# Kernel optimization log

Hardware: AMD Instinct MI355X
Metric: run time of the kernel (lower is better)

Reference implementation:

```python
import jax, jax.numpy as jnp
import numpy as np
from functools import partial

D_MODEL = 1024
D_HIDDEN = 4096
N_BLOCKS = 4
D_VOCAB = 32000
BATCH = 2
SEQ = 2048
LN_EPS = 1e-5
LRELU_SLOPE = 0.01  # torch nn.LeakyReLU default


def setup_inputs() -> dict:
    key = jax.random.key(0)
    ks = jax.random.split(key, 16)
    d, h, L, v = D_MODEL, D_HIDDEN, N_BLOCKS, D_VOCAB
    scale = d ** 0.5
    inp = {
        "tokens": jax.random.randint(ks[0], (BATCH, SEQ), 0, v, dtype=jnp.int64)
                  if jax.config.jax_enable_x64 else
                  jax.random.randint(ks[0], (BATCH, SEQ), 0, v, dtype=jnp.int32),
        "emb": jax.random.normal(ks[1], (v, d), jnp.float32) * 0.02,
        # per-block stacked params (leading axis = layer) for lax.scan
        "qk": jax.random.normal(ks[2], (L, d, d), jnp.float32) / scale,
        "ov": jax.random.normal(ks[3], (L, d, d), jnp.float32) / scale,
        "w_up": jax.random.normal(ks[4], (L, d, h), jnp.float32) / scale,
        "b_up": jnp.zeros((L, h), jnp.float32),
        "w_hid": jax.random.normal(ks[5], (L, h, h), jnp.float32) / (h ** 0.5),
        "b_hid": jnp.zeros((L, h), jnp.float32),
        "w_down": jax.random.normal(ks[6], (L, h, d), jnp.float32) / (h ** 0.5),
        "b_down": jnp.zeros((L, d), jnp.float32),
        "ln1_g": jnp.ones((L, d), jnp.float32),
        "ln1_b": jnp.zeros((L, d), jnp.float32),
        "ln2_g": jnp.ones((L, d), jnp.float32),
        "ln2_b": jnp.zeros((L, d), jnp.float32),
    }
    return inp


def _layer_norm(x, g, b):
    mu = jnp.mean(x, axis=-1, keepdims=True)
    var = jnp.mean(jnp.square(x - mu), axis=-1, keepdims=True)
    return (x - mu) * jax.lax.rsqrt(var + LN_EPS) * g + b


def _forward(tokens, emb, qk, ov, w_up, b_up, w_hid, b_hid, w_down, b_down,
             ln1_g, ln1_b, ln2_g, ln2_b):
    x = emb[tokens]                                   # [B, S, D]
    seq = tokens.shape[1]
    scale = jnp.asarray(D_MODEL ** 0.5, x.dtype)
    causal = jnp.tril(jnp.ones((seq, seq), bool))     # True = keep

    def block(x, p):
        (qk, ov, w_up, b_up, w_hid, b_hid, w_down, b_down,
         g1, b1, g2, b2) = p
        h = _layer_norm(x, g1, b1)
        # attention: (h @ qk @ h^T) / sqrt(d), causal mask, softmax, @ h @ ov
        scores = jnp.einsum('bsd,de,bte->bst', h, qk, h) / scale
        scores = jnp.where(causal, scores, -jnp.inf)
        attn = jax.nn.softmax(scores, axis=-1)
        x = x + jnp.einsum('bst,btd,de->bse', attn, h, ov)
        # MLP with LeakyReLU after every layer (incl. output)
        m = _layer_norm(x, g2, b2)
        m = jax.nn.leaky_relu(m @ w_up + b_up, LRELU_SLOPE)
        m = jax.nn.leaky_relu(m @ w_hid + b_hid, LRELU_SLOPE)
        m = jax.nn.leaky_relu(m @ w_down + b_down, LRELU_SLOPE)
        return x + m, None

    params = (qk, ov, w_up, b_up, w_hid, b_hid, w_down, b_down,
              ln1_g, ln1_b, ln2_g, ln2_b)
    x, _ = jax.lax.scan(block, x, params)
    return x @ emb.T                                  # [B, S, V] logits


@jax.jit
def reference(tokens, emb, qk, ov, w_up, b_up, w_hid, b_hid, w_down, b_down,
              ln1_g, ln1_b, ln2_g, ln2_b):
    return _forward(tokens, emb, qk, ov, w_up, b_up, w_hid, b_hid,
                    w_down, b_down, ln1_g, ln1_b, ln2_g, ln2_b)
```

## Files before the change

### kernel.cpp

```cpp
#include <hip/hip_runtime.h>

#define BS   4096
#define SEQL 2048
#define DM   1024
#define DH   4096
#define NV   32000

using u16 = unsigned short;

typedef __attribute__((ext_vector_type(8))) short bf16x8;
typedef __attribute__((ext_vector_type(4))) float f32x4;

__device__ __forceinline__ u16 f2b(float f) {
  union { float f; unsigned u; } c; c.f = f;
  unsigned u = c.u;
  u = (u + 0x7FFFu + ((u >> 16) & 1u)) >> 16;
  return (u16)u;
}

__device__ __forceinline__ void gld16(const u16* g, u16* l) {
  __builtin_amdgcn_global_load_lds(
      (__attribute__((address_space(1))) void*)(void*)const_cast<u16*>(g),
      (__attribute__((address_space(3))) void*)l, 16, 0, 0);
}

__global__ __launch_bounds__(256) void k_embed(const int* __restrict__ tok,
                                               const float* __restrict__ emb,
                                               float* __restrict__ x) {
  const long row = blockIdx.x;
  const long e = tok[row];
  ((float4*)(x + row * DM))[threadIdx.x] = ((const float4*)(emb + e * DM))[threadIdx.x];
}

__global__ __launch_bounds__(256) void k_cvt(const float* __restrict__ in,
                                             u16* __restrict__ out, int n4) {
  int i = blockIdx.x * 256 + threadIdx.x;
  if (i < n4) {
    float4 v = ((const float4*)in)[i];
    ushort4 o;
    o.x = f2b(v.x); o.y = f2b(v.y); o.z = f2b(v.z); o.w = f2b(v.w);
    ((ushort4*)out)[i] = o;
  }
}

__global__ __launch_bounds__(256) void k_ln(const float* __restrict__ x,
                                            const float* __restrict__ g,
                                            const float* __restrict__ b,
                                            u16* __restrict__ out) {
  const long row = blockIdx.x;
  const int t = threadIdx.x;
  float4 v = ((const float4*)(x + row * DM))[t];
  float s  = v.x + v.y + v.z + v.w;
  float q2 = v.x*v.x + v.y*v.y + v.z*v.z + v.w*v.w;
#pragma unroll
  for (int o = 1; o < 64; o <<= 1) { s += __shfl_xor(s, o); q2 += __shfl_xor(q2, o); }
  __shared__ float rs_[4], rq_[4];
  const int lane = t & 63, wid = t >> 6;
  if (lane == 0) { rs_[wid] = s; rq_[wid] = q2; }
  __syncthreads();
  s  = rs_[0] + rs_[1] + rs_[2] + rs_[3];
  q2 = rq_[0] + rq_[1] + rq_[2] + rq_[3];
  const float mu   = s * (1.f / 1024.f);
  const float var  = q2 * (1.f / 1024.f) - mu * mu;
  const float rstd = rsqrtf(var + 1e-5f);
  float4 gg = ((const float4*)g)[t];
  float4 bb = ((const float4*)b)[t];
  ushort4 o;
  o.x = f2b((v.x - mu) * rstd * gg.x + bb.x);
  o.y = f2b((v.y - mu) * rstd * gg.y + bb.y);
  o.z = f2b((v.z - mu) * rstd * gg.z + bb.z);
  o.w = f2b((v.w - mu) * rstd * gg.w + bb.w);
  ((ushort4*)(out + row * DM))[t] = o;
}

__device__ __forceinline__ u16 to_b16(float v) { return f2b(v); }
__device__ __forceinline__ u16 to_b16(u16 v)   { return v; }

template <typename T>
__global__ __launch_bounds__(256) void k_transpose(const T* __restrict__ in,
                                                   u16* __restrict__ out,
                                                   int R, int C, long inz, long outz) {
  __shared__ u16 tile[32][33];
  const T* ip = in + (long)blockIdx.z * inz;
  u16* op = out + (long)blockIdx.z * outz;
  const int tx = threadIdx.x & 31, ty = threadIdx.x >> 5;
  const long c0 = (long)blockIdx.x * 32, r0 = (long)blockIdx.y * 32;
#pragma unroll
  for (int i = 0; i < 4; ++i)
    tile[ty + i * 8][tx] = to_b16(ip[(r0 + ty + i * 8) * C + c0 + tx]);
  __syncthreads();
#pragma unroll
  for (int i = 0; i < 4; ++i)
    op[(c0 + ty + i * 8) * R + r0 + tx] = tile[tx][ty + i * 8];
}

__global__ __launch_bounds__(256) void k_softmax(const float* __restrict__ sc,
                                                 u16* __restrict__ at) {
  const int r = blockIdx.x;
  const long z = blockIdx.y;
  const int t = threadIdx.x;
  const float* row = sc + (z * SEQL + r) * SEQL;
  u16* orow = at + (z * SEQL + r) * SEQL;
  float vals[8];
  float mx = -3.4e38f;
#pragma unroll
  for (int i = 0; i < 8; ++i) {
    int c = i * 256 + t;
    float v = (c <= r) ? row[c] : -3.4e38f;
    vals[i] = v;
    mx = fmaxf(mx, v);
  }
#pragma unroll
  for (int o = 1; o < 64; o <<= 1) mx = fmaxf(mx, __shfl_xor(mx, o));
  __shared__ float rm[4], rsum[4];
  const int lane = t & 63, wid = t >> 6;
  if (lane == 0) rm[wid] = mx;
  __syncthreads();
  mx = fmaxf(fmaxf(rm[0], rm[1]), fmaxf(rm[2], rm[3]));
  float sum = 0.f;
#pragma unroll
  for (int i = 0; i < 8; ++i) {
    int c = i * 256 + t;
    float e = (c <= r) ? __expf(vals[i] - mx) : 0.f;
    vals[i] = e;
    sum += e;
  }
#pragma unroll
  for (int o = 1; o < 64; o <<= 1) sum += __shfl_xor(sum, o);
  if (lane == 0) rsum[wid] = sum;
  __syncthreads();
  sum = rsum[0] + rsum[1] + rsum[2] + rsum[3];
  const float inv = 1.f / sum;
#pragma unroll
  for (int i = 0; i < 8; ++i) orow[i * 256 + t] = f2b(vals[i] * inv);
}

template <int EPI, bool BIAS, bool LRELU, int CAUSAL>
__global__ __launch_bounds__(256, 2) void k_gemm_bt(
    const u16* __restrict__ A, const u16* __restrict__ B, void* __restrict__ C,
    const float* __restrict__ bias, int K, int N,
    long sAz, long sBz, long sCz, float scale) {
  __shared__ u16 lA[128 * 32];
  __shared__ u16 lB[128 * 32];
  const int t = threadIdx.x;
  const long z = blockIdx.z;
  const long row0 = (long)blockIdx.x * 128;
  const long col0 = (long)blockIdx.y * 128;
  if (CAUSAL == 1 && col0 > row0 + 127) return;
  const int Klim = (CAUSAL == 2) ? min(K, (int)row0 + 128) : K;
  const u16* Ab = A + z * sAz;
  const u16* Bb = B + z * sBz;

  const int rr = t >> 2;
  const int c8 = (t & 3) * 8;
  const u16* gA0 = Ab + (row0 + rr) * K + c8;
  const u16* gA1 = Ab + (row0 + 64 + rr) * K + c8;
  const u16* gB0 = Bb + (col0 + rr) * K + c8;
  const u16* gB1 = Bb + (col0 + 64 + rr) * K + c8;
  u16* sA0 = &lA[rr * 32 + c8];
  u16* sA1 = &lA[(64 + rr) * 32 + c8];
  u16* sB0 = &lB[rr * 32 + c8];
  u16* sB1 = &lB[(64 + rr) * 32 + c8];

  const int lane = t & 63;
  const int w = t >> 6;
  const int wr = (w >> 1) * 64, wc = (w & 1) * 64;
  const int fr = lane & 15;
  const int fk = (lane >> 4) * 8;

  f32x4 acc[4][4] = {};

  for (int k0 = 0; k0 < Klim; k0 += 32) {
    gld16(gA0 + k0, sA0);
    gld16(gA1 + k0, sA1);
    gld16(gB0 + k0, sB0);
    gld16(gB1 + k0, sB1);
    __syncthreads();
    bf16x8 av[4], bv[4];
#pragma unroll
    for (int m = 0; m < 4; ++m) av[m] = *(const bf16x8*)&lA[(wr + m * 16 + fr) * 32 + fk];
#pragma unroll
    for (int n = 0; n < 4; ++n) bv[n] = *(const bf16x8*)&lB[(wc + n * 16 + fr) * 32 + fk];
#pragma unroll
    for (int m = 0; m < 4; ++m)
#pragma unroll
      for (int n = 0; n < 4; ++n)
        acc[m][n] = __builtin_amdgcn_mfma_f32_16x16x32_bf16(av[m], bv[n], acc[m][n], 0, 0, 0);
    __syncthreads();
  }

  const int er = (lane >> 4) * 4;
  const int ec = lane & 15;
#pragma unroll
  for (int m = 0; m < 4; ++m) {
#pragma unroll
    for (int n = 0; n < 4; ++n) {
#pragma unroll
      for (int j = 0; j < 4; ++j) {
        long r = row0 + wr + m * 16 + er + j;
        long c = col0 + wc + n * 16 + ec;
        float v = acc[m][n][j] * scale;
        if (BIAS)  v += bias[c];
        if (LRELU) v = v > 0.f ? v : 0.01f * v;
        if (EPI == 0)      ((float*)C)[z * sCz + r * (long)N + c] = v;
        else if (EPI == 1) ((u16*)C)[z * sCz + r * (long)N + c] = f2b(v);
        else               ((float*)C)[z * sCz + r * (long)N + c] += v;
      }
    }
  }
}

template <int EPI, bool BIAS, bool LRELU>
__global__ __launch_bounds__(512, 1) void k_gemm256(
    const u16* __restrict__ A, const u16* __restrict__ B, void* __restrict__ C,
    const float* __restrict__ bias, int K, int N, float scale) {
  __shared__ u16 S[65536];
  char* Sc = (char*)&S[0];
  const int t = threadIdx.x;
  const int lane = t & 63;
  const int w = t >> 6;
  const int wr = w >> 2;
  const int wc = w & 3;
  const long row0 = (long)blockIdx.x * 256;
  const long col0 = (long)blockIdx.y * 256;
  const int nt = K >> 6;

  int srow[2], scol[2], ldsb[2];
#pragma unroll
  for (int i = 0; i < 2; ++i) {
    int d = t * 16 + i * 8192;
    int dx = d ^ (((d >> 7) & 3) << 4);
    srow[i] = dx >> 6;
    scol[i] = (dx & 63) >> 1;
    ldsb[i] = d;
  }
  const u16* Abase = A + row0 * (long)K;
  const u16* Bbase = B + col0 * (long)K;

  auto stage = [&](int opb, int kh, int buf, int kb) {
#pragma unroll
    for (int i = 0; i < 2; ++i) {
      const u16* src = (opb ? Bbase : Abase) + (long)srow[i] * K + kb + kh * 32 + scol[i];
      u16* dst = &S[(buf * 4 + opb * 2 + kh) * 8192 + (ldsb[i] >> 1)];
      gld16(src, dst);
    }
  };

  const int fr = lane & 15;
  const int fky = lane >> 4;
  const int axor = ((fr >> 1) & 3) << 4;
  int aoff[8], boff[4];
#pragma unroll
  for (int m = 0; m < 8; ++m)
    aoff[m] = (((wr * 128 + m * 16 + fr) * 64) + fky * 16) ^ axor;
#pragma unroll
  for (int n = 0; n < 4; ++n)
    boff[n] = (((wc * 64 + n * 16 + fr) * 64) + fky * 16) ^ axor;

  f32x4 acc[8][4] = {};

#define PHASE(kh, mh, sop, skh, guard, knext)                                    \
  {                                                                              \
    const char* Ah = Sc + cur * 65536 + (kh) * 16384;                            \
    const char* Bh = Sc + cur * 65536 + 32768 + (kh) * 16384;                    \
    bf16x8 av0 = *(const bf16x8*)(Ah + aoff[(mh) * 4 + 0]);                      \
    bf16x8 av1 = *(const bf16x8*)(Ah + aoff[(mh) * 4 + 1]);                      \
    bf16x8 av2 = *(const bf16x8*)(Ah + aoff[(mh) * 4 + 2]);                      \
    bf16x8 av3 = *(const bf16x8*)(Ah + aoff[(mh) * 4 + 3]);                      \
    bf16x8 bv0 = *(const bf16x8*)(Bh + boff[0]);                                 \
    bf16x8 bv1 = *(const bf16x8*)(Bh + boff[1]);                                 \
    bf16x8 bv2 = *(const bf16x8*)(Bh + boff[2]);                                 \
    bf16x8 bv3 = *(const bf16x8*)(Bh + boff[3]);                                 \
    stage(sop, skh, nxt, knext);                                                 \
    __builtin_amdgcn_s_barrier();                                                \
    __builtin_amdgcn_s_setprio(1);                                               \
    acc[(mh)*4+0][0] = __builtin_amdgcn_mfma_f32_16x16x32_bf16(av0, bv0, acc[(mh)*4+0][0], 0, 0, 0); \
    acc[(mh)*4+0][1] = __builtin_amdgcn_mfma_f32_16x16x32_bf16(av0, bv1, acc[(mh)*4+0][1], 0, 0, 0); \
    acc[(mh)*4+0][2] = __builtin_amdgcn_mfma_f32_16x16x32_bf16(av0, bv2, acc[(mh)*4+0][2], 0, 0, 0); \
    acc[(mh)*4+0][3] = __builtin_amdgcn_mfma_f32_16x16x32_bf16(av0, bv3, acc[(mh)*4+0][3], 0, 0, 0); \
    acc[(mh)*4+1][0] = __builtin_amdgcn_mfma_f32_16x16x32_bf16(av1, bv0, acc[(mh)*4+1][0], 0, 0, 0); \
    acc[(mh)*4+1][1] = __builtin_amdgcn_mfma_f32_16x16x32_bf16(av1, bv1, acc[(mh)*4+1][1], 0, 0, 0); \
    acc[(mh)*4+1][2] = __builtin_amdgcn_mfma_f32_16x16x32_bf16(av1, bv2, acc[(mh)*4+1][2], 0, 0, 0); \
    acc[(mh)*4+1][3] = __builtin_amdgcn_mfma_f32_16x16x32_bf16(av1, bv3, acc[(mh)*4+1][3], 0, 0, 0); \
    acc[(mh)*4+2][0] = __builtin_amdgcn_mfma_f32_16x16x32_bf16(av2, bv0, acc[(mh)*4+2][0], 0, 0, 0); \
    acc[(mh)*4+2][1] = __builtin_amdgcn_mfma_f32_16x16x32_bf16(av2, bv1, acc[(mh)*4+2][1], 0, 0, 0); \
    acc[(mh)*4+2][2] = __builtin_amdgcn_mfma_f32_16x16x32_bf16(av2, bv2, acc[(mh)*4+2][2], 0, 0, 0); \
    acc[(mh)*4+2][3] = __builtin_amdgcn_mfma_f32_16x16x32_bf16(av2, bv3, acc[(mh)*4+2][3], 0, 0, 0); \
    acc[(mh)*4+3][0] = __builtin_amdgcn_mfma_f32_16x16x32_bf16(av3, bv0, acc[(mh)*4+3][0], 0, 0, 0); \
    acc[(mh)*4+3][1] = __builtin_amdgcn_mfma_f32_16x16x32_bf16(av3, bv1, acc[(mh)*4+3][1], 0, 0, 0); \
    acc[(mh)*4+3][2] = __builtin_amdgcn_mfma_f32_16x16x32_bf16(av3, bv2, acc[(mh)*4+3][2], 0, 0, 0); \
    acc[(mh)*4+3][3] = __builtin_amdgcn_mfma_f32_16x16x32_bf16(av3, bv3, acc[(mh)*4+3][3], 0, 0, 0); \
    __builtin_amdgcn_s_setprio(0);                                               \
    if (guard) asm volatile("s_waitcnt vmcnt(4)" ::: "memory");                  \
    __builtin_amdgcn_s_barrier();                                                \
  }

  stage(0, 0, 0, 0);
  stage(1, 0, 0, 0);
  stage(0, 1, 0, 0);
  stage(1, 1, 0, 0);
  asm volatile("s_waitcnt vmcnt(4)" ::: "memory");
  __builtin_amdgcn_s_barrier();

  int cur = 0, nxt = 1;
  for (int tt = 0; tt < nt; ++tt) {
    const int knext = (tt + 1 < nt) ? (tt + 1) * 64 : tt * 64;
    PHASE(0, 0, 0, 0, false, knext)
    PHASE(0, 1, 1, 0, true,  knext)
    PHASE(1, 0, 0, 1, false, knext)
    PHASE(1, 1, 1, 1, true,  knext)
    cur ^= 1; nxt ^= 1;
  }
  asm volatile("s_waitcnt vmcnt(0)" ::: "memory");
#undef PHASE

  const int er = (lane >> 4) * 4;
  const int ec = lane & 15;
#pragma unroll
  for (int m = 0; m < 8; ++m) {
#pragma unroll
    for (int n = 0; n < 4; ++n) {
#pragma unroll
      for (int j = 0; j < 4; ++j) {
        long r = row0 + wr * 128 + m * 16 + er + j;
        long c = col0 + wc * 64 + n * 16 + ec;
        float v = acc[m][n][j] * scale;
        if (BIAS)  v += bias[c];
        if (LRELU) v = v > 0.f ? v : 0.01f * v;
        if (EPI == 0)      ((float*)C)[r * (long)N + c] = v;
        else if (EPI == 1) ((u16*)C)[r * (long)N + c] = f2b(v);
        else               ((float*)C)[r * (long)N + c] += v;
      }
    }
  }
}

extern "C" void kernel_launch(void* const* d_in, const int* in_sizes, int n_in,
                              void* d_out, int out_size, void* d_ws, size_t ws_size,
                              hipStream_t stream) {
  const int*   tokens = (const int*)d_in[0];
  const float* emb    = (const float*)d_in[1];
  const float* qk     = (const float*)d_in[2];
  const float* ov     = (const float*)d_in[3];
  const float* wup    = (const float*)d_in[4];
  const float* bup    = (const float*)d_in[5];
  const float* whid   = (const float*)d_in[6];
  const float* bhid   = (const float*)d_in[7];
  const float* wdown  = (const float*)d_in[8];
  const float* bdown  = (const float*)d_in[9];
  const float* g1     = (const float*)d_in[10];
  const float* b1     = (const float*)d_in[11];
  const float* g2     = (const float*)d_in[12];
  const float* b2     = (const float*)d_in[13];

  char* Ob = (char*)d_out;
  float* scores = (float*)(Ob + 0);
  u16*   attn   = (u16*)(Ob + 33554432);
  u16*   m1     = (u16*)(Ob + 50331648);
  u16*   m2     = (u16*)(Ob + 83886080);
  u16*   qkT    = (u16*)(Ob + 117440512);
  u16*   ovT    = (u16*)(Ob + 125829120);
  u16*   upT    = (u16*)(Ob + 134217728);
  u16*   hidT   = (u16*)(Ob + 167772160);
  u16*   downT  = (u16*)(Ob + 301989888);
  float* xres   = (float*)(Ob + 335544320);
  u16*   h      = (u16*)(Ob + 352321536);
  u16*   hT     = (u16*)(Ob + 360710144);
  u16*   q      = (u16*)(Ob + 369098752);
  u16*   attnV  = (u16*)(Ob + 377487360);

  u16* embB = (u16*)d_ws;
  u16* xB   = (u16*)((char*)d_ws + 65536000);

  k_embed<<<dim3(BS), 256, 0, stream>>>(tokens, emb, xres);
  k_cvt<<<dim3(32000), 256, 0, stream>>>(emb, embB, 8192000);

  k_transpose<float><<<dim3(32, 32, 4),   256, 0, stream>>>(qk,    qkT,   1024, 1024, 1048576,  1048576);
  k_transpose<float><<<dim3(32, 32, 4),   256, 0, stream>>>(ov,    ovT,   1024, 1024, 1048576,  1048576);
  k_transpose<float><<<dim3(128, 32, 4),  256, 0, stream>>>(wup,   upT,   1024, 4096, 4194304,  4194304);
  k_transpose<float><<<dim3(128, 128, 4), 256, 0, stream>>>(whid,  hidT,  4096, 4096, 16777216, 16777216);
  k_transpose<float><<<dim3(32, 128, 4),  256, 0, stream>>>(wdown, downT, 4096, 1024, 4194304,  4194304);

  for (int l = 0; l < 4; ++l) {
    k_ln<<<dim3(BS), 256, 0, stream>>>(xres, g1 + l * 1024, b1 + l * 1024, h);
    k_transpose<u16><<<dim3(32, 64, 2), 256, 0, stream>>>(h, hT, 2048, 1024, 2048L * 1024, 1024L * 2048);
    k_gemm_bt<1, false, false, 0><<<dim3(32, 8, 1), 256, 0, stream>>>(
        h, qkT + (long)l * 1048576, q, nullptr, 1024, 1024, 0, 0, 0, 0.03125f);
    k_gemm_bt<0, false, false, 1><<<dim3(16, 16, 2), 256, 0, stream>>>(
        q, h, scores, nullptr, 1024, 2048, 2048L * 1024, 2048L * 1024, 2048L * 2048, 1.f);
    k_softmax<<<dim3(2048, 2), 256, 0, stream>>>(scores, attn);
    k_gemm_bt<1, false, false, 2><<<dim3(16, 8, 2), 256, 0, stream>>>(
        attn, hT, attnV, nullptr, 2048, 1024, 2048L * 2048, 1024L * 2048, 2048L * 1024, 1.f);
    k_gemm_bt<2, false, false, 0><<<dim3(32, 8, 1), 256, 0, stream>>>(
        attnV, ovT + (long)l * 1048576, xres, nullptr, 1024, 1024, 0, 0, 0, 1.f);

    k_ln<<<dim3(BS), 256, 0, stream>>>(xres, g2 + l * 1024, b2 + l * 1024, h);
    k_gemm256<1, true, true><<<dim3(16, 16), 512, 0, stream>>>(
        h, upT + (long)l * 4194304, m1, bup + l * 4096, 1024, 4096, 1.f);
    k_gemm256<1, true, true><<<dim3(16, 16), 512, 0, stream>>>(
        m1, hidT + (long)l * 16777216, m2, bhid + l * 4096, 4096, 4096, 1.f);
    k_gemm_bt<2, true, true, 0><<<dim3(32, 8, 1), 256, 0, stream>>>(
        m2, downT + (long)l * 4194304, xres, bdown + l * 1024, 4096, 1024, 0, 0, 0, 1.f);
  }

  k_cvt<<<dim3(4096), 256, 0, stream>>>(xres, xB, 1048576);
  k_gemm256<0, false, false><<<dim3(16, 125), 512, 0, stream>>>(
      xB, embB, (float*)d_out, nullptr, 1024, 32000, 1.f);
}
```

Measured before the change: 2.171 ms.

## Software-pipeline LDS fragment reads ahead of MFMAs and trim causal softmax loop

```diff
diff --git a/kernel.cpp b/kernel.cpp
--- a/kernel.cpp
+++ b/kernel.cpp
@@ -101,10 +101,10 @@
   const int t = threadIdx.x;
   const float* row = sc + (z * SEQL + r) * SEQL;
   u16* orow = at + (z * SEQL + r) * SEQL;
+  const int ni = (r >> 8) + 1;
   float vals[8];
   float mx = -3.4e38f;
-#pragma unroll
-  for (int i = 0; i < 8; ++i) {
+  for (int i = 0; i < ni; ++i) {
     int c = i * 256 + t;
     float v = (c <= r) ? row[c] : -3.4e38f;
     vals[i] = v;
@@ -118,8 +118,7 @@
   __syncthreads();
   mx = fmaxf(fmaxf(rm[0], rm[1]), fmaxf(rm[2], rm[3]));
   float sum = 0.f;
-#pragma unroll
-  for (int i = 0; i < 8; ++i) {
+  for (int i = 0; i < ni; ++i) {
     int c = i * 256 + t;
     float e = (c <= r) ? __expf(vals[i] - mx) : 0.f;
     vals[i] = e;
@@ -131,8 +130,7 @@
   __syncthreads();
   sum = rsum[0] + rsum[1] + rsum[2] + rsum[3];
   const float inv = 1.f / sum;
-#pragma unroll
-  for (int i = 0; i < 8; ++i) orow[i * 256 + t] = f2b(vals[i] * inv);
+  for (int i = 0; i < ni; ++i) orow[i * 256 + t] = f2b(vals[i] * inv);
 }
 
 template <int EPI, bool BIAS, bool LRELU, int CAUSAL>
@@ -258,42 +256,40 @@
     boff[n] = (((wc * 64 + n * 16 + fr) * 64) + fky * 16) ^ axor;
 
   f32x4 acc[8][4] = {};
-
-#define PHASE(kh, mh, sop, skh, guard, knext)                                    \
-  {                                                                              \
-    const char* Ah = Sc + cur * 65536 + (kh) * 16384;                            \
-    const char* Bh = Sc + cur * 65536 + 32768 + (kh) * 16384;                    \
-    bf16x8 av0 = *(const bf16x8*)(Ah + aoff[(mh) * 4 + 0]);                      \
-    bf16x8 av1 = *(const bf16x8*)(Ah + aoff[(mh) * 4 + 1]);                      \
-    bf16x8 av2 = *(const bf16x8*)(Ah + aoff[(mh) * 4 + 2]);                      \
-    bf16x8 av3 = *(const bf16x8*)(Ah + aoff[(mh) * 4 + 3]);                      \
-    bf16x8 bv0 = *(const bf16x8*)(Bh + boff[0]);                                 \
-    bf16x8 bv1 = *(const bf16x8*)(Bh + boff[1]);                                 \
-    bf16x8 bv2 = *(const bf16x8*)(Bh + boff[2]);                                 \
-    bf16x8 bv3 = *(const bf16x8*)(Bh + boff[3]);                                 \
-    stage(sop, skh, nxt, knext);                                                 \
-    __builtin_amdgcn_s_barrier();                                                \
-    __builtin_amdgcn_s_setprio(1);                                               \
-    acc[(mh)*4+0][0] = __builtin_amdgcn_mfma_f32_16x16x32_bf16(av0, bv0, acc[(mh)*4+0][0], 0, 0, 0); \
-    acc[(mh)*4+0][1] = __builtin_amdgcn_mfma_f32_16x16x32_bf16(av0, bv1, acc[(mh)*4+0][1], 0, 0, 0); \
-    acc[(mh)*4+0][2] = __builtin_amdgcn_mfma_f32_16x16x32_bf16(av0, bv2, acc[(mh)*4+0][2], 0, 0, 0); \
-    acc[(mh)*4+0][3] = __builtin_amdgcn_mfma_f32_16x16x32_bf16(av0, bv3, acc[(mh)*4+0][3], 0, 0, 0); \
-    acc[(mh)*4+1][0] = __builtin_amdgcn_mfma_f32_16x16x32_bf16(av1, bv0, acc[(mh)*4+1][0], 0, 0, 0); \
-    acc[(mh)*4+1][1] = __builtin_amdgcn_mfma_f32_16x16x32_bf16(av1, bv1, acc[(mh)*4+1][1], 0, 0, 0); \
-    acc[(mh)*4+1][2] = __builtin_amdgcn_mfma_f32_16x16x32_bf16(av1, bv2, acc[(mh)*4+1][2], 0, 0, 0); \
-    acc[(mh)*4+1][3] = __builtin_amdgcn_mfma_f32_16x16x32_bf16(av1, bv3, acc[(mh)*4+1][3], 0, 0, 0); \
-    acc[(mh)*4+2][0] = __builtin_amdgcn_mfma_f32_16x16x32_bf16(av2, bv0, acc[(mh)*4+2][0], 0, 0, 0); \
-    acc[(mh)*4+2][1] = __builtin_amdgcn_mfma_f32_16x16x32_bf16(av2, bv1, acc[(mh)*4+2][1], 0, 0, 0); \
-    acc[(mh)*4+2][2] = __builtin_amdgcn_mfma_f32_16x16x32_bf16(av2, bv2, acc[(mh)*4+2][2], 0, 0, 0); \
-    acc[(mh)*4+2][3] = __builtin_amdgcn_mfma_f32_16x16x32_bf16(av2, bv3, acc[(mh)*4+2][3], 0, 0, 0); \
-    acc[(mh)*4+3][0] = __builtin_amdgcn_mfma_f32_16x16x32_bf16(av3, bv0, acc[(mh)*4+3][0], 0, 0, 0); \
-    acc[(mh)*4+3][1] = __builtin_amdgcn_mfma_f32_16x16x32_bf16(av3, bv1, acc[(mh)*4+3][1], 0, 0, 0); \
-    acc[(mh)*4+3][2] = __builtin_amdgcn_mfma_f32_16x16x32_bf16(av3, bv2, acc[(mh)*4+3][2], 0, 0, 0); \
-    acc[(mh)*4+3][3] = __builtin_amdgcn_mfma_f32_16x16x32_bf16(av3, bv3, acc[(mh)*4+3][3], 0, 0, 0); \
-    __builtin_amdgcn_s_setprio(0);                                               \
-    if (guard) asm volatile("s_waitcnt vmcnt(4)" ::: "memory");                  \
-    __builtin_amdgcn_s_barrier();                                                \
-  }
+  bf16x8 aA0, aA1, aA2, aA3, aB0, aB1, aB2, aB3;
+  bf16x8 bX0, bX1, bX2, bX3, bY0, bY1, bY2, bY3;
+
+#define RD_A(d0, d1, d2, d3, bb, kh, mh)                                   \
+  { const char* Ah_ = Sc + (bb) * 65536 + (kh) * 16384;                    \
+    d0 = *(const bf16x8*)(Ah_ + aoff[(mh) * 4 + 0]);                       \
+    d1 = *(const bf16x8*)(Ah_ + aoff[(mh) * 4 + 1]);                       \
+    d2 = *(const bf16x8*)(Ah_ + aoff[(mh) * 4 + 2]);                       \
+    d3 = *(const bf16x8*)(Ah_ + aoff[(mh) * 4 + 3]); }
+#define RD_B(d0, d1, d2, d3, bb, kh)                                       \
+  { const char* Bh_ = Sc + (bb) * 65536 + 32768 + (kh) * 16384;            \
+    d0 = *(const bf16x8*)(Bh_ + boff[0]);                                  \
+    d1 = *(const bf16x8*)(Bh_ + boff[1]);                                  \
+    d2 = *(const bf16x8*)(Bh_ + boff[2]);                                  \
+    d3 = *(const bf16x8*)(Bh_ + boff[3]); }
+#define MF16(a0, a1, a2, a3, b0, b1, b2, b3, mh)                                                     \
+  __builtin_amdgcn_s_setprio(1);                                                                     \
+  acc[(mh)*4+0][0] = __builtin_amdgcn_mfma_f32_16x16x32_bf16(a0, b0, acc[(mh)*4+0][0], 0, 0, 0);     \
+  acc[(mh)*4+0][1] = __builtin_amdgcn_mfma_f32_16x16x32_bf16(a0, b1, acc[(mh)*4+0][1], 0, 0, 0);     \
+  acc[(mh)*4+0][2] = __builtin_amdgcn_mfma_f32_16x16x32_bf16(a0, b2, acc[(mh)*4+0][2], 0, 0, 0);     \
+  acc[(mh)*4+0][3] = __builtin_amdgcn_mfma_f32_16x16x32_bf16(a0, b3, acc[(mh)*4+0][3], 0, 0, 0);     \
+  acc[(mh)*4+1][0] = __builtin_amdgcn_mfma_f32_16x16x32_bf16(a1, b0, acc[(mh)*4+1][0], 0, 0, 0);     \
+  acc[(mh)*4+1][1] = __builtin_amdgcn_mfma_f32_16x16x32_bf16(a1, b1, acc[(mh)*4+1][1], 0, 0, 0);     \
+  acc[(mh)*4+1][2] = __builtin_amdgcn_mfma_f32_16x16x32_bf16(a1, b2, acc[(mh)*4+1][2], 0, 0, 0);     \
+  acc[(mh)*4+1][3] = __builtin_amdgcn_mfma_f32_16x16x32_bf16(a1, b3, acc[(mh)*4+1][3], 0, 0, 0);     \
+  acc[(mh)*4+2][0] = __builtin_amdgcn_mfma_f32_16x16x32_bf16(a2, b0, acc[(mh)*4+2][0], 0, 0, 0);     \
+  acc[(mh)*4+2][1] = __builtin_amdgcn_mfma_f32_16x16x32_bf16(a2, b1, acc[(mh)*4+2][1], 0, 0, 0);     \
+  acc[(mh)*4+2][2] = __builtin_amdgcn_mfma_f32_16x16x32_bf16(a2, b2, acc[(mh)*4+2][2], 0, 0, 0);     \
+  acc[(mh)*4+2][3] = __builtin_amdgcn_mfma_f32_16x16x32_bf16(a2, b3, acc[(mh)*4+2][3], 0, 0, 0);     \
+  acc[(mh)*4+3][0] = __builtin_amdgcn_mfma_f32_16x16x32_bf16(a3, b0, acc[(mh)*4+3][0], 0, 0, 0);     \
+  acc[(mh)*4+3][1] = __builtin_amdgcn_mfma_f32_16x16x32_bf16(a3, b1, acc[(mh)*4+3][1], 0, 0, 0);     \
+  acc[(mh)*4+3][2] = __builtin_amdgcn_mfma_f32_16x16x32_bf16(a3, b2, acc[(mh)*4+3][2], 0, 0, 0);     \
+  acc[(mh)*4+3][3] = __builtin_amdgcn_mfma_f32_16x16x32_bf16(a3, b3, acc[(mh)*4+3][3], 0, 0, 0);     \
+  __builtin_amdgcn_s_setprio(0);
 
   stage(0, 0, 0, 0);
   stage(1, 0, 0, 0);
@@ -301,18 +297,39 @@
   stage(1, 1, 0, 0);
   asm volatile("s_waitcnt vmcnt(4)" ::: "memory");
   __builtin_amdgcn_s_barrier();
-
-  int cur = 0, nxt = 1;
+  RD_A(aA0, aA1, aA2, aA3, 0, 0, 0);
+  RD_B(bX0, bX1, bX2, bX3, 0, 0);
+
+  int cur = 0;
   for (int tt = 0; tt < nt; ++tt) {
-    const int knext = (tt + 1 < nt) ? (tt + 1) * 64 : tt * 64;
-    PHASE(0, 0, 0, 0, false, knext)
-    PHASE(0, 1, 1, 0, true,  knext)
-    PHASE(1, 0, 0, 1, false, knext)
-    PHASE(1, 1, 1, 1, true,  knext)
-    cur ^= 1; nxt ^= 1;
+    const int knext = (tt + 1 < nt ? tt + 1 : tt) * 64;
+    const int nx = cur ^ 1;
+    RD_A(aB0, aB1, aB2, aB3, cur, 0, 1);
+    stage(0, 0, nx, knext);
+    MF16(aA0, aA1, aA2, aA3, bX0, bX1, bX2, bX3, 0);
+    asm volatile("s_waitcnt vmcnt(2)" ::: "memory");
+    __builtin_amdgcn_s_barrier();
+    RD_A(aA0, aA1, aA2, aA3, cur, 1, 0);
+    RD_B(bY0, bY1, bY2, bY3, cur, 1);
+    stage(1, 0, nx, knext);
+    MF16(aB0, aB1, aB2, aB3, bX0, bX1, bX2, bX3, 1);
+    __builtin_amdgcn_s_barrier();
+    RD_A(aB0, aB1, aB2, aB3, cur, 1, 1);
+    stage(0, 1, nx, knext);
+    MF16(aA0, aA1, aA2, aA3, bY0, bY1, bY2, bY3, 0);
+    asm volatile("s_waitcnt vmcnt(2)" ::: "memory");
+    __builtin_amdgcn_s_barrier();
+    RD_A(aA0, aA1, aA2, aA3, nx, 0, 0);
+    RD_B(bX0, bX1, bX2, bX3, nx, 0);
+    stage(1, 1, nx, knext);
+    MF16(aB0, aB1, aB2, aB3, bY0, bY1, bY2, bY3, 1);
+    __builtin_amdgcn_s_barrier();
+    cur = nx;
   }
   asm volatile("s_waitcnt vmcnt(0)" ::: "memory");
-#undef PHASE
+#undef RD_A
+#undef RD_B
+#undef MF16
 
   const int er = (lane >> 4) * 4;
   const int ec = lane & 15;
```

Measured after the change: 2.181 ms. Within noise of the previous version (+0.5%).
